# Kernel optimization log

Measured on AMD Instinct MI355X. Metric: run time of the kernel, lower is better.

Reference implementation:

```python
import jax, jax.numpy as jnp
import numpy as np

# Faithful JAX translation of Decoder.forward in mode='train' (teacher forcing).
# Dropout is treated as eval-mode identity (deterministic reference).
# PyTorch GRU gate order in W_ih/W_hh is (r, z, n).

def setup_inputs() -> dict:
    key = jax.random.key(0)
    ks = jax.random.split(key, 12)
    B, S, H = 32, 50, 1024      # H = dim_hidden*2
    V, Dw, T = 32000, 512, 32   # vocab, dim_word, max_len
    Din = H + Dw                # GRU input size
    s = 0.02
    return {
        'encoder_outputs': jax.random.normal(ks[0], (B, S, H), jnp.float32),
        'encoder_hidden':  jax.random.normal(ks[1], (1, B, H), jnp.float32),
        'targets':         jax.random.randint(ks[2], (B, T), 0, V),
        'emb':     jax.random.normal(ks[3], (V, Dw), jnp.float32) * s,
        'attn_W1': jax.random.normal(ks[4], (H, 2 * H), jnp.float32) * s,
        'attn_b1': jnp.zeros((H,), jnp.float32),
        'attn_W2': jax.random.normal(ks[5], (1, H), jnp.float32) * s,
        'W_ih':    jax.random.normal(ks[6], (3 * H, Din), jnp.float32) * s,
        'b_ih':    jnp.zeros((3 * H,), jnp.float32),
        'W_hh':    jax.random.normal(ks[7], (3 * H, H), jnp.float32) * s,
        'b_hh':    jnp.zeros((3 * H,), jnp.float32),
        'W_out':   jax.random.normal(ks[8], (V, H), jnp.float32) * s,
        'b_out':   jnp.zeros((V,), jnp.float32),
    }


def _attention(h, enc, W1, b1, W2):
    # h: [B,H], enc: [B,S,H] -> context [B,H]
    B, S, H = enc.shape
    hcat = jnp.concatenate([enc, jnp.broadcast_to(h[:, None, :], (B, S, H))], axis=-1)  # [B,S,2H]
    aw = jnp.tanh(jnp.einsum('bsd,kd->bsk', hcat, W1) + b1)          # [B,S,H]
    e = jnp.einsum('bsk,ok->bso', aw, W2)[..., 0]                    # [B,S]
    alpha = jax.nn.softmax(e, axis=1)
    return jnp.einsum('bs,bsh->bh', alpha, enc)


def _gru_cell(x, h, W_ih, b_ih, W_hh, b_hh):
    H = h.shape[-1]
    gi = x @ W_ih.T + b_ih   # [B,3H]
    gh = h @ W_hh.T + b_hh
    i_r, i_z, i_n = gi[:, :H], gi[:, H:2*H], gi[:, 2*H:]
    h_r, h_z, h_n = gh[:, :H], gh[:, H:2*H], gh[:, 2*H:]
    r = jax.nn.sigmoid(i_r + h_r)
    z = jax.nn.sigmoid(i_z + h_z)
    n = jnp.tanh(i_n + r * h_n)
    return (1.0 - z) * n + z * h


def reference(encoder_outputs, encoder_hidden, targets, emb, attn_W1, attn_b1,
              attn_W2, W_ih, b_ih, W_hh, b_hh, W_out, b_out):
    h0 = encoder_hidden[0]                   # [B,H] (n_layers=1, unidirectional)
    T = targets.shape[1]
    targets_emb = emb[targets]               # [B,T,Dw]
    xs = jnp.swapaxes(targets_emb[:, :T - 1, :], 0, 1)  # [T-1,B,Dw]

    def step(h, x_t):
        context = _attention(h, encoder_outputs, attn_W1, attn_b1, attn_W2)
        dec_in = jnp.concatenate([x_t, context], axis=1)   # [B, Dw+H]
        h_new = _gru_cell(dec_in, h, W_ih, b_ih, W_hh, b_hh)
        logprobs = jax.nn.log_softmax(h_new @ W_out.T + b_out, axis=1)
        return h_new, logprobs

    _, logps = jax.lax.scan(step, h0, xs)    # [T-1,B,V]
    return jnp.swapaxes(logps, 0, 1)         # [B,T-1,V]
```

## Files before the change

### kernel.cpp

```cpp
#include <hip/hip_runtime.h>
#include <stdint.h>

typedef unsigned short u16;
typedef __bf16 bf16x8 __attribute__((ext_vector_type(8)));
typedef float  f32x4  __attribute__((ext_vector_type(4)));

static __device__ __forceinline__ u16 f2bf(float x){
  uint32_t u = __float_as_uint(x);
  u += 0x7fffu + ((u >> 16) & 1u);
  return (u16)(u >> 16);
}

__global__ __launch_bounds__(256) void conv_bf16_k(const float* __restrict__ src,
                                                   u16* __restrict__ dst, int n4){
  int i = blockIdx.x * 256 + threadIdx.x;
  int stride = gridDim.x * 256;
  for (; i < n4; i += stride){
    float4 v = ((const float4*)src)[i];
    ushort4 o;
    o.x = f2bf(v.x); o.y = f2bf(v.y); o.z = f2bf(v.z); o.w = f2bf(v.w);
    ((ushort4*)dst)[i] = o;
  }
}

__global__ __launch_bounds__(128) void embed_k(const int* __restrict__ targets,
                                               const float* __restrict__ emb,
                                               const float* __restrict__ ench,
                                               float* __restrict__ xemb,
                                               float* __restrict__ h0){
  int blk = blockIdx.x;
  if (blk < 992){
    int t = blk >> 5, b = blk & 31;
    int tok = targets[b * 32 + t];
    const float4* src = (const float4*)(emb + (size_t)tok * 512);
    float4* dst = (float4*)(xemb + (size_t)blk * 512);
    dst[threadIdx.x] = src[threadIdx.x];
  } else {
    int i = (blk - 992) * 128 + threadIdx.x;
    ((float4*)h0)[i] = ((const float4*)ench)[i];
  }
}

__global__ __launch_bounds__(256) void gemm_f32_k(const float* __restrict__ A,
                                                  const float* __restrict__ B,
                                                  const float* __restrict__ bias,
                                                  float* __restrict__ C,
                                                  int M, int K, int lda, int ldb, int ldc){
  __shared__ float As[16 * 72];
  __shared__ float Bs[16 * 72];
  int tid = threadIdx.x;
  int m0 = blockIdx.y * 64, n0 = blockIdx.x * 64;
  int tx = tid & 15, ty = tid >> 4;
  int lrow = tid >> 2, lk = (tid & 3) * 4;
  const float* Ap = A + (size_t)(m0 + lrow) * lda + lk;
  const float* Bp = B + (size_t)(n0 + lrow) * ldb + lk;
  bool avalid = (m0 + lrow) < M;
  float acc[4][4] = {};
  for (int k0 = 0; k0 < K; k0 += 16){
    float4 av = avalid ? *(const float4*)(Ap + k0) : float4{0.f,0.f,0.f,0.f};
    float4 bv = *(const float4*)(Bp + k0);
    __syncthreads();
    As[(lk+0)*72 + lrow] = av.x; As[(lk+1)*72 + lrow] = av.y;
    As[(lk+2)*72 + lrow] = av.z; As[(lk+3)*72 + lrow] = av.w;
    Bs[(lk+0)*72 + lrow] = bv.x; Bs[(lk+1)*72 + lrow] = bv.y;
    Bs[(lk+2)*72 + lrow] = bv.z; Bs[(lk+3)*72 + lrow] = bv.w;
    __syncthreads();
#pragma unroll
    for (int kk = 0; kk < 16; ++kk){
      float4 a = *(const float4*)&As[kk*72 + ty*4];
      float4 b = *(const float4*)&Bs[kk*72 + tx*4];
      float avv[4] = {a.x, a.y, a.z, a.w};
      float bvv[4] = {b.x, b.y, b.z, b.w};
#pragma unroll
      for (int i = 0; i < 4; ++i)
#pragma unroll
        for (int j = 0; j < 4; ++j)
          acc[i][j] = fmaf(avv[i], bvv[j], acc[i][j]);
    }
  }
  float4 bb = *(const float4*)(bias + n0 + tx*4);
#pragma unroll
  for (int i = 0; i < 4; ++i){
    int row = m0 + ty*4 + i;
    if (row < M){
      float4 o;
      o.x = acc[i][0] + bb.x; o.y = acc[i][1] + bb.y;
      o.z = acc[i][2] + bb.z; o.w = acc[i][3] + bb.w;
      *(float4*)(C + (size_t)row * ldc + n0 + tx*4) = o;
    }
  }
}

__global__ __launch_bounds__(256) void hproj_k(const float* __restrict__ h,
                                               const float* __restrict__ W1,
                                               float* __restrict__ hp){
  int b = threadIdx.x & 31, kk = threadIdx.x >> 5;
  int k = blockIdx.x * 8 + kk;
  const float4* hr = (const float4*)(h + b * 1024);
  const float4* wr = (const float4*)(W1 + (size_t)k * 2048 + 1024);
  float acc = 0.f;
  for (int d = 0; d < 256; ++d){
    float4 a = hr[d], w = wr[d];
    acc = fmaf(a.x, w.x, fmaf(a.y, w.y, fmaf(a.z, w.z, fmaf(a.w, w.w, acc))));
  }
  hp[b * 1024 + k] = acc;
}

__global__ __launch_bounds__(256) void attn_k(const float* __restrict__ ep,
                                              const float* __restrict__ hp,
                                              const float* __restrict__ W2,
                                              const float* __restrict__ enc,
                                              float* __restrict__ ctx){
  __shared__ float hp_s[1024];
  __shared__ float w2_s[1024];
  __shared__ float e_s[50];
  int b = blockIdx.x;
  int tid = threadIdx.x, lane = tid & 63, w = tid >> 6;
  ((float4*)hp_s)[tid] = ((const float4*)(hp + b * 1024))[tid];
  ((float4*)w2_s)[tid] = ((const float4*)W2)[tid];
  __syncthreads();
  for (int s = w; s < 50; s += 4){
    const float* eprow = ep + (size_t)(b * 50 + s) * 1024;
    float v = 0.f;
#pragma unroll
    for (int kx = 0; kx < 16; ++kx){
      int k = lane + kx * 64;
      v += tanhf(eprow[k] + hp_s[k]) * w2_s[k];
    }
    for (int off = 32; off; off >>= 1) v += __shfl_xor(v, off);
    if (lane == 0) e_s[s] = v;
  }
  __syncthreads();
  float m = -1e30f;
  for (int s = 0; s < 50; ++s) m = fmaxf(m, e_s[s]);
  float sum = 0.f;
  for (int s = 0; s < 50; ++s) sum += expf(e_s[s] - m);
  float inv = 1.f / sum;
  float4 c = {0.f,0.f,0.f,0.f};
  const float4* encb = (const float4*)(enc + (size_t)b * 50 * 1024);
  for (int s = 0; s < 50; ++s){
    float a = expf(e_s[s] - m) * inv;
    float4 ev = encb[s * 256 + tid];
    c.x = fmaf(a, ev.x, c.x); c.y = fmaf(a, ev.y, c.y);
    c.z = fmaf(a, ev.z, c.z); c.w = fmaf(a, ev.w, c.w);
  }
  ((float4*)(ctx + b * 1024))[tid] = c;
}

__global__ __launch_bounds__(256) void gru_k(const float* __restrict__ h,
                                             const float* __restrict__ ctx,
                                             const float* __restrict__ Wih,
                                             const float* __restrict__ Whh,
                                             const float* __restrict__ bhh,
                                             const float* __restrict__ gix_t,
                                             float* __restrict__ hnew){
  int b = threadIdx.x & 31, jj = threadIdx.x >> 5;
  int j = blockIdx.x * 8 + jj;
  const float4* hr = (const float4*)(h + b * 1024);
  const float4* cr = (const float4*)(ctx + b * 1024);
  const float4* wir = (const float4*)(Wih + (size_t)j * 1536 + 512);
  const float4* wiz = (const float4*)(Wih + (size_t)(1024 + j) * 1536 + 512);
  const float4* win = (const float4*)(Wih + (size_t)(2048 + j) * 1536 + 512);
  const float4* whr = (const float4*)(Whh + (size_t)j * 1024);
  const float4* whz = (const float4*)(Whh + (size_t)(1024 + j) * 1024);
  const float4* whn = (const float4*)(Whh + (size_t)(2048 + j) * 1024);
  float ar=0.f, az=0.f, an=0.f, br=0.f, bz=0.f, bn=0.f;
  for (int d = 0; d < 256; ++d){
    float4 cv = cr[d], hv = hr[d], w;
    w = wir[d]; ar += cv.x*w.x + cv.y*w.y + cv.z*w.z + cv.w*w.w;
    w = wiz[d]; az += cv.x*w.x + cv.y*w.y + cv.z*w.z + cv.w*w.w;
    w = win[d]; an += cv.x*w.x + cv.y*w.y + cv.z*w.z + cv.w*w.w;
    w = whr[d]; br += hv.x*w.x + hv.y*w.y + hv.z*w.z + hv.w*w.w;
    w = whz[d]; bz += hv.x*w.x + hv.y*w.y + hv.z*w.z + hv.w*w.w;
    w = whn[d]; bn += hv.x*w.x + hv.y*w.y + hv.z*w.z + hv.w*w.w;
  }
  float ir  = ar + gix_t[b * 3072 + j];
  float iz  = az + gix_t[b * 3072 + 1024 + j];
  float inn = an + gix_t[b * 3072 + 2048 + j];
  float hr_ = br + bhh[j];
  float hz_ = bz + bhh[1024 + j];
  float hn_ = bn + bhh[2048 + j];
  float r = 1.f / (1.f + expf(-(ir + hr_)));
  float z = 1.f / (1.f + expf(-(iz + hz_)));
  float n = tanhf(inn + r * hn_);
  float hv = h[b * 1024 + j];
  hnew[b * 1024 + j] = (1.f - z) * n + z * hv;
}

__global__ __launch_bounds__(256) void logits_k(const u16* __restrict__ Abf,
                                                const u16* __restrict__ Wbf,
                                                const float* __restrict__ bout,
                                                float* __restrict__ out){
  __shared__ u16 As[64 * 40];
  int tid = threadIdx.x, lane = tid & 63, w = tid >> 6;
  int n0 = blockIdx.x * 64, m0 = blockIdx.y * 64;
  int lr = tid >> 2, lk = (tid & 3) * 8;
  int r16 = lane & 15, kq = lane >> 4;
  bool avalid = (m0 + lr) < 992;
  const uint4* Ap = (const uint4*)(Abf + (size_t)(m0 + lr) * 1024 + lk);
  const uint4* Wp = (const uint4*)(Wbf + (size_t)(n0 + w * 16 + r16) * 1024 + kq * 8);
  f32x4 acc0 = {0.f,0.f,0.f,0.f}, acc1 = {0.f,0.f,0.f,0.f};
  f32x4 acc2 = {0.f,0.f,0.f,0.f}, acc3 = {0.f,0.f,0.f,0.f};
  for (int k0 = 0; k0 < 1024; k0 += 32){
    uint4 a4 = avalid ? Ap[k0 >> 3] : uint4{0,0,0,0};
    uint4 b4 = Wp[k0 >> 3];
    __syncthreads();
    *(uint4*)&As[lr * 40 + lk] = a4;
    __syncthreads();
    bf16x8 bfr = __builtin_bit_cast(bf16x8, b4);
    bf16x8 a0 = __builtin_bit_cast(bf16x8, *(const uint4*)&As[( 0 + r16) * 40 + kq * 8]);
    acc0 = __builtin_amdgcn_mfma_f32_16x16x32_bf16(a0, bfr, acc0, 0, 0, 0);
    bf16x8 a1 = __builtin_bit_cast(bf16x8, *(const uint4*)&As[(16 + r16) * 40 + kq * 8]);
    acc1 = __builtin_amdgcn_mfma_f32_16x16x32_bf16(a1, bfr, acc1, 0, 0, 0);
    bf16x8 a2 = __builtin_bit_cast(bf16x8, *(const uint4*)&As[(32 + r16) * 40 + kq * 8]);
    acc2 = __builtin_amdgcn_mfma_f32_16x16x32_bf16(a2, bfr, acc2, 0, 0, 0);
    bf16x8 a3 = __builtin_bit_cast(bf16x8, *(const uint4*)&As[(48 + r16) * 40 + kq * 8]);
    acc3 = __builtin_amdgcn_mfma_f32_16x16x32_bf16(a3, bfr, acc3, 0, 0, 0);
  }
  int n = n0 + w * 16 + r16;
  float bo = bout[n];
#define STORE_MS(MS, ACC)                                                        \
  {                                                                              \
    _Pragma("unroll")                                                            \
    for (int reg = 0; reg < 4; ++reg){                                           \
      int m = m0 + MS * 16 + kq * 4 + reg;                                       \
      if (m < 992){                                                              \
        int tt = m >> 5, bb = m & 31;                                            \
        out[(size_t)(bb * 31 + tt) * 32000 + n] = ACC[reg] + bo;                 \
      }                                                                          \
    }                                                                            \
  }
  STORE_MS(0, acc0) STORE_MS(1, acc1) STORE_MS(2, acc2) STORE_MS(3, acc3)
#undef STORE_MS
}

__global__ __launch_bounds__(256) void lsm_k(float* __restrict__ out){
  __shared__ float red[4];
  __shared__ float red2[4];
  int row = blockIdx.x, tid = threadIdx.x, w = tid >> 6;
  float* p = out + (size_t)row * 32000;
  const float4* p4 = (const float4*)p;
  float m = -1e30f;
  for (int i = tid; i < 8000; i += 256){
    float4 v = p4[i];
    m = fmaxf(m, fmaxf(fmaxf(v.x, v.y), fmaxf(v.z, v.w)));
  }
  for (int off = 32; off; off >>= 1) m = fmaxf(m, __shfl_xor(m, off));
  if ((tid & 63) == 0) red[w] = m;
  __syncthreads();
  m = fmaxf(fmaxf(red[0], red[1]), fmaxf(red[2], red[3]));
  float s = 0.f;
  for (int i = tid; i < 8000; i += 256){
    float4 v = p4[i];
    s += expf(v.x - m) + expf(v.y - m) + expf(v.z - m) + expf(v.w - m);
  }
  for (int off = 32; off; off >>= 1) s += __shfl_xor(s, off);
  if ((tid & 63) == 0) red2[w] = s;
  __syncthreads();
  s = red2[0] + red2[1] + red2[2] + red2[3];
  float lse = m + logf(s);
  for (int i = tid; i < 8000; i += 256){
    float4 v = p4[i];
    v.x -= lse; v.y -= lse; v.z -= lse; v.w -= lse;
    ((float4*)p)[i] = v;
  }
}

extern "C" void kernel_launch(void* const* d_in, const int* in_sizes, int n_in,
                              void* d_out, int out_size, void* d_ws, size_t ws_size,
                              hipStream_t stream){
  const float* enc  = (const float*)d_in[0];
  const float* ench = (const float*)d_in[1];
  const int*   tgt  = (const int*)d_in[2];
  const float* emb  = (const float*)d_in[3];
  const float* W1   = (const float*)d_in[4];
  const float* b1   = (const float*)d_in[5];
  const float* W2   = (const float*)d_in[6];
  const float* Wih  = (const float*)d_in[7];
  const float* bih  = (const float*)d_in[8];
  const float* Whh  = (const float*)d_in[9];
  const float* bhh  = (const float*)d_in[10];
  const float* Wout = (const float*)d_in[11];
  const float* bout = (const float*)d_in[12];
  float* out = (float*)d_out;

  char* ws = (char*)d_ws;
  size_t off = 0;
  auto alloc = [&](size_t bytes)->char*{
    char* p = ws + off;
    off += (bytes + 255) & ~(size_t)255;
    return p;
  };
  float* EP   = (float*)alloc((size_t)1600 * 1024 * 4);
  float* GIX  = (float*)alloc((size_t)992 * 3072 * 4);
  float* XEMB = (float*)alloc((size_t)992 * 512 * 4);
  float* HBUF = (float*)alloc((size_t)32 * 32 * 1024 * 4);
  float* HP   = (float*)alloc((size_t)32 * 1024 * 4);
  float* CTX  = (float*)alloc((size_t)32 * 1024 * 4);
  u16*   WBF  = (u16*)alloc((size_t)32000 * 1024 * 2);
  u16*   ABF  = (u16*)alloc((size_t)992 * 1024 * 2);
  (void)ws_size; (void)in_sizes; (void)n_in; (void)out_size;

  conv_bf16_k<<<2048, 256, 0, stream>>>(Wout, WBF, 32000 * 1024 / 4);
  embed_k<<<1056, 128, 0, stream>>>(tgt, emb, ench, XEMB, HBUF);
  gemm_f32_k<<<dim3(16, 25), 256, 0, stream>>>(enc, W1, b1, EP, 1600, 1024, 1024, 2048, 1024);
  gemm_f32_k<<<dim3(48, 16), 256, 0, stream>>>(XEMB, Wih, bih, GIX, 992, 512, 512, 1536, 3072);

  for (int t = 0; t < 31; ++t){
    const float* h = HBUF + (size_t)t * 32768;
    hproj_k<<<128, 256, 0, stream>>>(h, W1, HP);
    attn_k<<<32, 256, 0, stream>>>(EP, HP, W2, enc, CTX);
    gru_k<<<128, 256, 0, stream>>>(h, CTX, Wih, Whh, bhh,
                                   GIX + (size_t)t * 32 * 3072,
                                   HBUF + (size_t)(t + 1) * 32768);
  }

  conv_bf16_k<<<1024, 256, 0, stream>>>(HBUF + 32768, ABF, 992 * 1024 / 4);
  logits_k<<<dim3(500, 16), 256, 0, stream>>>(ABF, WBF, bout, out);
  lsm_k<<<992, 256, 0, stream>>>(out);
}
```

Before: 7.665 ms.

## Fuse recurrent decoder loop into one persistent kernel with grid barriers

```diff
diff --git a/kernel.cpp b/kernel.cpp
--- a/kernel.cpp
+++ b/kernel.cpp
@@ -9,6 +9,16 @@
   uint32_t u = __float_as_uint(x);
   u += 0x7fffu + ((u >> 16) & 1u);
   return (u16)(u >> 16);
+}
+static __device__ __forceinline__ float dot4(float4 a, float4 b){
+  return a.x*b.x + a.y*b.y + a.z*b.z + a.w*b.w;
+}
+static __device__ __forceinline__ float ftanh(float x){
+  float e = __expf(2.f*x);
+  return 1.f - 2.f/(e + 1.f);
+}
+static __device__ __forceinline__ float fsigm(float x){
+  return 1.f / (1.f + __expf(-x));
 }
 
 __global__ __launch_bounds__(256) void conv_bf16_k(const float* __restrict__ src,
@@ -91,100 +101,198 @@
   }
 }
 
-__global__ __launch_bounds__(256) void hproj_k(const float* __restrict__ h,
-                                               const float* __restrict__ W1,
-                                               float* __restrict__ hp){
-  int b = threadIdx.x & 31, kk = threadIdx.x >> 5;
-  int k = blockIdx.x * 8 + kk;
-  const float4* hr = (const float4*)(h + b * 1024);
-  const float4* wr = (const float4*)(W1 + (size_t)k * 2048 + 1024);
-  float acc = 0.f;
-  for (int d = 0; d < 256; ++d){
-    float4 a = hr[d], w = wr[d];
-    acc = fmaf(a.x, w.x, fmaf(a.y, w.y, fmaf(a.z, w.z, fmaf(a.w, w.w, acc))));
-  }
-  hp[b * 1024 + k] = acc;
-}
-
-__global__ __launch_bounds__(256) void attn_k(const float* __restrict__ ep,
-                                              const float* __restrict__ hp,
-                                              const float* __restrict__ W2,
-                                              const float* __restrict__ enc,
-                                              float* __restrict__ ctx){
-  __shared__ float hp_s[1024];
-  __shared__ float w2_s[1024];
-  __shared__ float e_s[50];
-  int b = blockIdx.x;
-  int tid = threadIdx.x, lane = tid & 63, w = tid >> 6;
-  ((float4*)hp_s)[tid] = ((const float4*)(hp + b * 1024))[tid];
-  ((float4*)w2_s)[tid] = ((const float4*)W2)[tid];
+static __device__ __forceinline__ void gridbar(unsigned* bar, unsigned* gen,
+                                               unsigned &mygen, int nblk){
   __syncthreads();
-  for (int s = w; s < 50; s += 4){
-    const float* eprow = ep + (size_t)(b * 50 + s) * 1024;
-    float v = 0.f;
-#pragma unroll
-    for (int kx = 0; kx < 16; ++kx){
-      int k = lane + kx * 64;
-      v += tanhf(eprow[k] + hp_s[k]) * w2_s[k];
-    }
-    for (int off = 32; off; off >>= 1) v += __shfl_xor(v, off);
-    if (lane == 0) e_s[s] = v;
+  if (threadIdx.x == 0){
+    __threadfence();
+    unsigned g = mygen;
+    unsigned old = __hip_atomic_fetch_add(bar, 1u, __ATOMIC_ACQ_REL,
+                                          __HIP_MEMORY_SCOPE_AGENT);
+    if (old == (unsigned)(nblk - 1)){
+      __hip_atomic_store(bar, 0u, __ATOMIC_RELAXED, __HIP_MEMORY_SCOPE_AGENT);
+      __hip_atomic_fetch_add(gen, 1u, __ATOMIC_RELEASE, __HIP_MEMORY_SCOPE_AGENT);
+    } else {
+      int spins = 0;
+      while (__hip_atomic_load(gen, __ATOMIC_ACQUIRE, __HIP_MEMORY_SCOPE_AGENT) <= g){
+        __builtin_amdgcn_s_sleep(8);
+        if (++spins > (1 << 15)) break;
+      }
+    }
   }
   __syncthreads();
-  float m = -1e30f;
-  for (int s = 0; s < 50; ++s) m = fmaxf(m, e_s[s]);
-  float sum = 0.f;
-  for (int s = 0; s < 50; ++s) sum += expf(e_s[s] - m);
-  float inv = 1.f / sum;
-  float4 c = {0.f,0.f,0.f,0.f};
-  const float4* encb = (const float4*)(enc + (size_t)b * 50 * 1024);
-  for (int s = 0; s < 50; ++s){
-    float a = expf(e_s[s] - m) * inv;
-    float4 ev = encb[s * 256 + tid];
-    c.x = fmaf(a, ev.x, c.x); c.y = fmaf(a, ev.y, c.y);
-    c.z = fmaf(a, ev.z, c.z); c.w = fmaf(a, ev.w, c.w);
-  }
-  ((float4*)(ctx + b * 1024))[tid] = c;
-}
-
-__global__ __launch_bounds__(256) void gru_k(const float* __restrict__ h,
-                                             const float* __restrict__ ctx,
-                                             const float* __restrict__ Wih,
-                                             const float* __restrict__ Whh,
-                                             const float* __restrict__ bhh,
-                                             const float* __restrict__ gix_t,
-                                             float* __restrict__ hnew){
-  int b = threadIdx.x & 31, jj = threadIdx.x >> 5;
-  int j = blockIdx.x * 8 + jj;
-  const float4* hr = (const float4*)(h + b * 1024);
-  const float4* cr = (const float4*)(ctx + b * 1024);
-  const float4* wir = (const float4*)(Wih + (size_t)j * 1536 + 512);
-  const float4* wiz = (const float4*)(Wih + (size_t)(1024 + j) * 1536 + 512);
-  const float4* win = (const float4*)(Wih + (size_t)(2048 + j) * 1536 + 512);
-  const float4* whr = (const float4*)(Whh + (size_t)j * 1024);
-  const float4* whz = (const float4*)(Whh + (size_t)(1024 + j) * 1024);
-  const float4* whn = (const float4*)(Whh + (size_t)(2048 + j) * 1024);
-  float ar=0.f, az=0.f, an=0.f, br=0.f, bz=0.f, bn=0.f;
-  for (int d = 0; d < 256; ++d){
-    float4 cv = cr[d], hv = hr[d], w;
-    w = wir[d]; ar += cv.x*w.x + cv.y*w.y + cv.z*w.z + cv.w*w.w;
-    w = wiz[d]; az += cv.x*w.x + cv.y*w.y + cv.z*w.z + cv.w*w.w;
-    w = win[d]; an += cv.x*w.x + cv.y*w.y + cv.z*w.z + cv.w*w.w;
-    w = whr[d]; br += hv.x*w.x + hv.y*w.y + hv.z*w.z + hv.w*w.w;
-    w = whz[d]; bz += hv.x*w.x + hv.y*w.y + hv.z*w.z + hv.w*w.w;
-    w = whn[d]; bn += hv.x*w.x + hv.y*w.y + hv.z*w.z + hv.w*w.w;
-  }
-  float ir  = ar + gix_t[b * 3072 + j];
-  float iz  = az + gix_t[b * 3072 + 1024 + j];
-  float inn = an + gix_t[b * 3072 + 2048 + j];
-  float hr_ = br + bhh[j];
-  float hz_ = bz + bhh[1024 + j];
-  float hn_ = bn + bhh[2048 + j];
-  float r = 1.f / (1.f + expf(-(ir + hr_)));
-  float z = 1.f / (1.f + expf(-(iz + hz_)));
-  float n = tanhf(inn + r * hn_);
-  float hv = h[b * 1024 + j];
-  hnew[b * 1024 + j] = (1.f - z) * n + z * hv;
+  mygen++;
+}
+
+__global__ __launch_bounds__(512, 2) void persist_k(
+    const float* __restrict__ enc, const float* __restrict__ W1,
+    const float* __restrict__ W2, const float* __restrict__ Wih,
+    const float* __restrict__ Whh, const float* __restrict__ bhh,
+    const float* __restrict__ EP, const float* __restrict__ GIX,
+    float* __restrict__ HBUF, float* __restrict__ HP,
+    float* __restrict__ CTX, unsigned* __restrict__ BAR){
+  __shared__ float sPart[8 * 50 + 64];
+  int tid = threadIdx.x, bid = blockIdx.x;
+  unsigned* bar = BAR;
+  unsigned* gen = BAR + 32;
+  unsigned mygen = 0;
+
+  int q = tid & 7, dq = (tid >> 3) & 3, bq = tid >> 5;
+  int b0 = bq * 2, b1 = b0 + 1;
+  int lane31 = tid & 31;
+
+  float2 w2r = *(const float2*)&W2[(tid & 511) * 2 < 1024 ? tid * 2 : 0];
+  float bhhR[4][3];
+#pragma unroll
+  for (int jj = 0; jj < 4; ++jj){
+    int j = bid * 4 + jj;
+    bhhR[jj][0] = bhh[j]; bhhR[jj][1] = bhh[1024 + j]; bhhR[jj][2] = bhh[2048 + j];
+  }
+
+  for (int t = 0; t < 31; ++t){
+    const float* h = HBUF + (size_t)t * 32768;
+    float4 hA[8], hB[8];
+    {
+      const float4* h4 = (const float4*)h;
+#pragma unroll
+      for (int i = 0; i < 8; ++i){
+        int f = q + 8*dq + 32*i;
+        hA[i] = h4[b0*256 + f];
+        hB[i] = h4[b1*256 + f];
+      }
+    }
+    {
+      float a0[4], a1[4];
+#pragma unroll
+      for (int kk = 0; kk < 4; ++kk){
+        int k = bid*4 + kk;
+        const float4* wr = (const float4*)(W1 + (size_t)k*2048 + 1024);
+        float s0 = 0.f, s1 = 0.f;
+#pragma unroll
+        for (int i = 0; i < 8; ++i){
+          int f = q + 8*dq + 32*i;
+          float4 w = wr[f];
+          s0 += dot4(w, hA[i]); s1 += dot4(w, hB[i]);
+        }
+        a0[kk] = s0; a1[kk] = s1;
+      }
+#pragma unroll
+      for (int kk = 0; kk < 4; ++kk)
+        for (int o = 1; o < 32; o <<= 1){
+          a0[kk] += __shfl_xor(a0[kk], o);
+          a1[kk] += __shfl_xor(a1[kk], o);
+        }
+      if (lane31 == 0){
+#pragma unroll
+        for (int kk = 0; kk < 4; ++kk){
+          HP[b0*1024 + bid*4 + kk] = a0[kk];
+          HP[b1*1024 + bid*4 + kk] = a1[kk];
+        }
+      }
+    }
+    gridbar(bar, gen, mygen, 256);
+
+    if (bid < 32){
+      int b = bid;
+      float2 hp2 = *(const float2*)&HP[b*1024 + tid*2];
+      int lane = tid & 63, wv = tid >> 6;
+      for (int s = 0; s < 50; ++s){
+        float2 ep2 = *(const float2*)&EP[(size_t)(b*50 + s)*1024 + tid*2];
+        float v = ftanh(ep2.x + hp2.x) * w2r.x + ftanh(ep2.y + hp2.y) * w2r.y;
+        for (int o = 32; o; o >>= 1) v += __shfl_xor(v, o);
+        if (lane == 0) sPart[s*8 + wv] = v;
+      }
+      __syncthreads();
+      if (tid < 64){
+        float e = -1e30f;
+        if (tid < 50){
+          e = 0.f;
+#pragma unroll
+          for (int p = 0; p < 8; ++p) e += sPart[tid*8 + p];
+        }
+        float mx = e;
+        for (int o = 32; o; o >>= 1) mx = fmaxf(mx, __shfl_xor(mx, o));
+        float ex = (tid < 50) ? __expf(e - mx) : 0.f;
+        float sm = ex;
+        for (int o = 32; o; o >>= 1) sm += __shfl_xor(sm, o);
+        if (tid < 50) sPart[400 + tid] = ex / sm;
+      }
+      __syncthreads();
+      float cx = 0.f, cy = 0.f;
+      const float* encb = enc + (size_t)b * 51200 + tid*2;
+      for (int s = 0; s < 50; ++s){
+        float a = sPart[400 + s];
+        float2 ev = *(const float2*)&encb[s*1024];
+        cx = fmaf(a, ev.x, cx); cy = fmaf(a, ev.y, cy);
+      }
+      *(float2*)&CTX[b*1024 + tid*2] = float2{cx, cy};
+    }
+    gridbar(bar, gen, mygen, 256);
+
+    float4 cA[8], cB[8];
+    {
+      const float4* c4 = (const float4*)CTX;
+#pragma unroll
+      for (int i = 0; i < 8; ++i){
+        int f = q + 8*dq + 32*i;
+        cA[i] = c4[b0*256 + f];
+        cB[i] = c4[b1*256 + f];
+      }
+    }
+#pragma unroll
+    for (int jj = 0; jj < 4; ++jj){
+      int j = bid*4 + jj;
+      const float4* wir = (const float4*)(Wih + (size_t)j*1536 + 512);
+      const float4* wiz = (const float4*)(Wih + (size_t)(1024 + j)*1536 + 512);
+      const float4* win = (const float4*)(Wih + (size_t)(2048 + j)*1536 + 512);
+      const float4* vhr = (const float4*)(Whh + (size_t)j*1024);
+      const float4* vhz = (const float4*)(Whh + (size_t)(1024 + j)*1024);
+      const float4* vhn = (const float4*)(Whh + (size_t)(2048 + j)*1024);
+      float air0=0, air1=0, aiz0=0, aiz1=0, ain0=0, ain1=0;
+      float bhr0=0, bhr1=0, bhz0=0, bhz1=0, bhn0=0, bhn1=0;
+#pragma unroll
+      for (int i = 0; i < 8; ++i){
+        int f = q + 8*dq + 32*i;
+        float4 w;
+        w = wir[f]; air0 += dot4(w, cA[i]); air1 += dot4(w, cB[i]);
+        w = wiz[f]; aiz0 += dot4(w, cA[i]); aiz1 += dot4(w, cB[i]);
+        w = win[f]; ain0 += dot4(w, cA[i]); ain1 += dot4(w, cB[i]);
+        w = vhr[f]; bhr0 += dot4(w, hA[i]); bhr1 += dot4(w, hB[i]);
+        w = vhz[f]; bhz0 += dot4(w, hA[i]); bhz1 += dot4(w, hB[i]);
+        w = vhn[f]; bhn0 += dot4(w, hA[i]); bhn1 += dot4(w, hB[i]);
+      }
+      for (int o = 1; o < 32; o <<= 1){
+        air0 += __shfl_xor(air0, o); air1 += __shfl_xor(air1, o);
+        aiz0 += __shfl_xor(aiz0, o); aiz1 += __shfl_xor(aiz1, o);
+        ain0 += __shfl_xor(ain0, o); ain1 += __shfl_xor(ain1, o);
+        bhr0 += __shfl_xor(bhr0, o); bhr1 += __shfl_xor(bhr1, o);
+        bhz0 += __shfl_xor(bhz0, o); bhz1 += __shfl_xor(bhz1, o);
+        bhn0 += __shfl_xor(bhn0, o); bhn1 += __shfl_xor(bhn1, o);
+      }
+      if (lane31 == 0){
+        float* hout = HBUF + (size_t)(t+1)*32768;
+#pragma unroll
+        for (int bb = 0; bb < 2; ++bb){
+          int b = (bb == 0) ? b0 : b1;
+          float ai_r = bb ? air1 : air0, ai_z = bb ? aiz1 : aiz0, ai_n = bb ? ain1 : ain0;
+          float ah_r = bb ? bhr1 : bhr0, ah_z = bb ? bhz1 : bhz0, ah_n = bb ? bhn1 : bhn0;
+          const float* gix = GIX + ((size_t)t*32 + b)*3072;
+          float ir  = ai_r + gix[j];
+          float iz  = ai_z + gix[1024 + j];
+          float in_ = ai_n + gix[2048 + j];
+          float hr_ = ah_r + bhhR[jj][0];
+          float hz_ = ah_z + bhhR[jj][1];
+          float hn_ = ah_n + bhhR[jj][2];
+          float r = fsigm(ir + hr_);
+          float z = fsigm(iz + hz_);
+          float n = ftanh(in_ + r * hn_);
+          float hv = h[b*1024 + j];
+          hout[b*1024 + j] = (1.f - z)*n + z*hv;
+        }
+      }
+    }
+    gridbar(bar, gen, mygen, 256);
+  }
 }
 
 __global__ __launch_bounds__(256) void logits_k(const u16* __restrict__ Abf,
@@ -252,13 +360,13 @@
   float s = 0.f;
   for (int i = tid; i < 8000; i += 256){
     float4 v = p4[i];
-    s += expf(v.x - m) + expf(v.y - m) + expf(v.z - m) + expf(v.w - m);
+    s += __expf(v.x - m) + __expf(v.y - m) + __expf(v.z - m) + __expf(v.w - m);
   }
   for (int off = 32; off; off >>= 1) s += __shfl_xor(s, off);
   if ((tid & 63) == 0) red2[w] = s;
   __syncthreads();
   s = red2[0] + red2[1] + red2[2] + red2[3];
-  float lse = m + logf(s);
+  float lse = m + __logf(s);
   for (int i = tid; i < 8000; i += 256){
     float4 v = p4[i];
     v.x -= lse; v.y -= lse; v.z -= lse; v.w -= lse;
@@ -299,6 +407,7 @@
   float* CTX  = (float*)alloc((size_t)32 * 1024 * 4);
   u16*   WBF  = (u16*)alloc((size_t)32000 * 1024 * 2);
   u16*   ABF  = (u16*)alloc((size_t)992 * 1024 * 2);
+  unsigned* BAR = (unsigned*)alloc(256);
   (void)ws_size; (void)in_sizes; (void)n_in; (void)out_size;
 
   conv_bf16_k<<<2048, 256, 0, stream>>>(Wout, WBF, 32000 * 1024 / 4);
@@ -306,14 +415,9 @@
   gemm_f32_k<<<dim3(16, 25), 256, 0, stream>>>(enc, W1, b1, EP, 1600, 1024, 1024, 2048, 1024);
   gemm_f32_k<<<dim3(48, 16), 256, 0, stream>>>(XEMB, Wih, bih, GIX, 992, 512, 512, 1536, 3072);
 
-  for (int t = 0; t < 31; ++t){
-    const float* h = HBUF + (size_t)t * 32768;
-    hproj_k<<<128, 256, 0, stream>>>(h, W1, HP);
-    attn_k<<<32, 256, 0, stream>>>(EP, HP, W2, enc, CTX);
-    gru_k<<<128, 256, 0, stream>>>(h, CTX, Wih, Whh, bhh,
-                                   GIX + (size_t)t * 32 * 3072,
-                                   HBUF + (size_t)(t + 1) * 32768);
-  }
+  hipMemsetAsync(BAR, 0, 256, stream);
+  persist_k<<<256, 512, 0, stream>>>(enc, W1, W2, Wih, Whh, bhh,
+                                     EP, GIX, HBUF, HP, CTX, BAR);
 
   conv_bf16_k<<<1024, 256, 0, stream>>>(HBUF + 32768, ABF, 992 * 1024 / 4);
   logits_k<<<dim3(500, 16), 256, 0, stream>>>(ABF, WBF, bout, out);
```

Result: slower. 14.85 ms (+93.7%).
